# Optimization experiments

Hardware: AMD Instinct MI355X
Metric: run time of the kernel (lower is better)

The kernel has to match this reference:

```python
import jax, jax.numpy as jnp
import numpy as np

B, S, D_MODEL, H = 2, 2048, 1024, 16
HD = D_MODEL // H  # head_dim = 64


def setup_inputs() -> dict:
    key = jax.random.key(0)
    kx, kq, kk, kv, ko = jax.random.split(key, 5)
    scale = 1.0 / np.sqrt(D_MODEL)
    return {
        "x": jax.random.normal(kx, (B, S, D_MODEL), dtype=jnp.float32),
        "Wq": jax.random.normal(kq, (D_MODEL, D_MODEL), dtype=jnp.float32) * scale,
        "Wk": jax.random.normal(kk, (D_MODEL, D_MODEL), dtype=jnp.float32) * scale,
        "Wv": jax.random.normal(kv, (D_MODEL, D_MODEL), dtype=jnp.float32) * scale,
        "Wo": jax.random.normal(ko, (D_MODEL, D_MODEL), dtype=jnp.float32) * scale,
        "bo": jnp.zeros((D_MODEL,), dtype=jnp.float32),
    }


def reference(x, Wq, Wk, Wv, Wo, bo):
    b, s, _ = x.shape
    # project and split heads: [b, h, s, hd]
    q = (x @ Wq).reshape(b, s, H, HD).transpose(0, 2, 1, 3)
    k = (x @ Wk).reshape(b, s, H, HD).transpose(0, 2, 1, 3)
    v = (x @ Wv).reshape(b, s, H, HD).transpose(0, 2, 1, 3)
    # full attn score materialization, as in the original module
    scores = jnp.einsum("bhqd,bhkd->bhqk", q, k)
    causal = jnp.triu(jnp.ones((s, s), dtype=bool), k=1)  # True above diagonal -> masked
    scores = jnp.where(causal, -jnp.inf, scores)
    attn = jax.nn.softmax(scores / np.sqrt(HD), axis=-1)  # dropout p=0.0 (eval)
    ctx = jnp.einsum("bhqk,bhkd->bqhd", attn, v).reshape(b, s, D_MODEL)
    return ctx @ Wo + bo
```

## Files before the change

kernel.cpp:

```cpp
#include <hip/hip_runtime.h>
#include <stdint.h>

typedef __bf16 bf16x8 __attribute__((ext_vector_type(8)));
typedef float f32x4 __attribute__((ext_vector_type(4)));

static constexpr int B_ = 2, S_ = 2048, D_ = 1024, H_ = 16, HD_ = 64;
static constexpr int M_ = B_ * S_;
static constexpr size_t HSZ = (size_t)B_ * H_ * S_ * HD_;

#define DEV_INLINE __device__ __forceinline__

#define SC2F (0.125f * 1.4426950408889634f)

DEV_INLINE uint16_t f2bf(float f) {
  __bf16 h = (__bf16)f;
  return __builtin_bit_cast(uint16_t, h);
}
DEV_INLINE float bf2f(uint16_t u) {
  uint32_t x = (uint32_t)u << 16;
  return __builtin_bit_cast(float, x);
}
DEV_INLINE float fmax3(float a, float b, float c) { return fmaxf(fmaxf(a, b), c); }

#define GLD16(gptr, lptr)                                                        \
  __builtin_amdgcn_global_load_lds(                                              \
      (const __attribute__((address_space(1))) void*)(gptr),                     \
      (__attribute__((address_space(3))) void*)(lptr), 16, 0, 0)

__global__ void cvt_x_kernel(const float* __restrict__ x, uint16_t* __restrict__ xb) {
  int i = blockIdx.x * 256 + threadIdx.x;
  float4 v = reinterpret_cast<const float4*>(x)[i];
  ushort4 o;
  o.x = f2bf(v.x); o.y = f2bf(v.y); o.z = f2bf(v.z); o.w = f2bf(v.w);
  reinterpret_cast<ushort4*>(xb)[i] = o;
}

__global__ void tr_w_kernel(const float* __restrict__ W0, const float* __restrict__ W1,
                            const float* __restrict__ W2, const float* __restrict__ W3,
                            uint16_t* __restrict__ Wt) {
  __shared__ float tile[32][33];
  const float* W = (blockIdx.z == 0) ? W0 : (blockIdx.z == 1) ? W1
                   : (blockIdx.z == 2) ? W2 : W3;
  uint16_t* dst = Wt + (size_t)blockIdx.z * D_ * D_;
  int c = blockIdx.x * 32 + threadIdx.x;
  int r0 = blockIdx.y * 32;
#pragma unroll
  for (int j = threadIdx.y; j < 32; j += 8)
    tile[j][threadIdx.x] = W[(size_t)(r0 + j) * D_ + c];
  __syncthreads();
  int oc = blockIdx.y * 32 + threadIdx.x;
  int or0 = blockIdx.x * 32;
#pragma unroll
  for (int j = threadIdx.y; j < 32; j += 8)
    dst[(size_t)(or0 + j) * D_ + oc] = f2bf(tile[threadIdx.x][j]);
}

template <int EPI, int BM, int MINW>
__global__ __launch_bounds__(256, MINW)
void gemm_bt_kernel(const uint16_t* __restrict__ A, const uint16_t* __restrict__ Bt,
                    uint16_t* __restrict__ Cb, float* __restrict__ Cf,
                    const float* __restrict__ bias, int K, int gx, int chunk) {
  constexpr int MR = BM / 32;
  __shared__ uint16_t ldsA[2][BM * 32];
  __shared__ uint16_t ldsB[2][128 * 32];
  const int tid = threadIdx.x;
  const int lane = tid & 63;
  const int wid = tid >> 6;
  const int lo = lane & 15, hi = lane >> 4;

  const int id = blockIdx.x;
  const int tilei = (id & 7) * chunk + (id >> 3);
  const int bx = tilei % gx, by = tilei / gx;
  const int row0 = by * BM, col0 = bx * 128;
  const int wr = (wid >> 1) * (BM / 2), wc = (wid & 1) * 64;

  const uint16_t* gA = A + (size_t)(row0 + (tid >> 2)) * K + (tid & 3) * 8;
  const uint16_t* gB = Bt + (size_t)(col0 + (tid >> 2)) * K + (tid & 3) * 8;

  f32x4 acc[MR][4] = {};

  auto stage = [&](int kt, int buf) {
    const uint16_t* a = gA + kt * 32;
    const uint16_t* b = gB + kt * 32;
    char* la = (char*)&ldsA[buf][0] + tid * 16;
    char* lb = (char*)&ldsB[buf][0] + tid * 16;
    GLD16(a, la);
    if constexpr (BM == 128) GLD16(a + (size_t)64 * K, la + 4096);
    GLD16(b, lb);
    GLD16(b + (size_t)64 * K, lb + 4096);
  };

  const int nk = K >> 5;
  stage(0, 0);
  __syncthreads();
  for (int kt = 0; kt < nk; ++kt) {
    const int cur = kt & 1;
    if (kt + 1 < nk) stage(kt + 1, cur ^ 1);
    const uint16_t* lA = &ldsA[cur][0];
    const uint16_t* lB = &ldsB[cur][0];
    bf16x8 af[MR], bfr[4];
#pragma unroll
    for (int m = 0; m < MR; ++m)
      af[m] = *(const bf16x8*)(lA + (wr + m * 16 + lo) * 32 + hi * 8);
#pragma unroll
    for (int n = 0; n < 4; ++n)
      bfr[n] = *(const bf16x8*)(lB + (wc + n * 16 + lo) * 32 + hi * 8);
    __builtin_amdgcn_s_setprio(1);
#pragma unroll
    for (int m = 0; m < MR; ++m)
#pragma unroll
      for (int n = 0; n < 4; ++n)
        acc[m][n] = __builtin_amdgcn_mfma_f32_16x16x32_bf16(af[m], bfr[n], acc[m][n], 0, 0, 0);
    __builtin_amdgcn_s_setprio(0);
    __syncthreads();
  }

#pragma unroll
  for (int m = 0; m < MR; ++m)
#pragma unroll
    for (int n = 0; n < 4; ++n) {
      const int gr0 = row0 + wr + m * 16 + hi * 4;
      const int gc = col0 + wc + n * 16 + lo;
      if (EPI == 0) {
        const int which = gc >> 10, c = gc & 1023;
        const int hh = c >> 6, d = c & 63;
        const int bb = gr0 >> 11, s0 = gr0 & 2047;
        if (which == 2) {
          ushort4 pk;
          pk.x = f2bf(acc[m][n][0]); pk.y = f2bf(acc[m][n][1]);
          pk.z = f2bf(acc[m][n][2]); pk.w = f2bf(acc[m][n][3]);
          *reinterpret_cast<ushort4*>(
              &Cb[2 * HSZ + ((size_t)(bb * H_ + hh) * HD_ + d) * S_ + s0]) = pk;
        } else {
          const float qs = (which == 0) ? SC2F : 1.0f;
#pragma unroll
          for (int j = 0; j < 4; ++j)
            Cb[(size_t)which * HSZ + (((size_t)(bb * H_ + hh) * S_ + s0 + j) * HD_ + d)] =
                f2bf(acc[m][n][j] * qs);
        }
      } else {
#pragma unroll
        for (int j = 0; j < 4; ++j)
          Cf[(size_t)(gr0 + j) * D_ + gc] = acc[m][n][j] + bias[gc];
      }
    }
}

__global__ __launch_bounds__(256, 3)
void attn_kernel(const uint16_t* __restrict__ QKV, uint16_t* __restrict__ ctx,
                 uint16_t* __restrict__ Opart, float2* __restrict__ ml) {
  __shared__ uint16_t ldsKV[2][2][4096];
  __shared__ uint16_t ldsP[128][72];

  static const uint8_t jt[3][8] = {
      {0 << 2, 1 << 2, 2 << 2, 3 << 2, 4 << 2, 5 << 2, 6 << 2, (9 << 2) | 3},
      {(15 << 2) | 2, 7 << 2, (14 << 2) | 2, (14 << 2) | 3,
       (13 << 2) | 3, (12 << 2) | 3, (10 << 2) | 3, (11 << 2) | 2},
      {(15 << 2) | 3, (13 << 2) | 2, (12 << 2) | 2, (10 << 2) | 2,
       (9 << 2) | 2, (8 << 2) | 2, (8 << 2) | 3, (11 << 2) | 3},
  };

  const int tid = threadIdx.x;
  const int lane = tid & 63;
  const int w = tid >> 6;
  const int lo = lane & 15, hi = lane >> 4;
  const int swz = (hi * 8) ^ ((lo & 6) << 2);

  const int g = blockIdx.x;
  const int bh = g & 31, k = (g >> 5) & 7, r = g >> 8;
  const int j = jt[r][k];
  const int p = j >> 2;
  const bool split = (j & 2) != 0;
  const int c = j & 1;
  const int k0 = (split && c) ? (p + 1) : 0;
  const int k1 = (split && !c) ? (p + 1) : (2 * p + 2);
  const int h = bh & 15, b = bh >> 4;

  const size_t bhs = ((size_t)(b * H_ + h)) * S_ * HD_;
  const uint16_t* Q  = QKV + bhs;
  const uint16_t* Kp = QKV + HSZ + bhs;
  const uint16_t* Vt = QKV + 2 * HSZ + bhs;

  bf16x8 ones;
#pragma unroll
  for (int e = 0; e < 8; ++e) ones[e] = __builtin_bit_cast(__bf16, (uint16_t)0x3F80);

  const int srow = tid >> 2;
  const int scol = ((tid & 3) ^ ((tid >> 3) & 3)) * 8;
  auto stage = [&](int kt, int bufi) {
    const uint16_t* gk = Kp + (size_t)(kt * 64 + srow) * HD_ + scol;
    char* lk = (char*)&ldsKV[bufi][0][0] + tid * 16;
    GLD16(gk, lk);
    GLD16(gk + 32, lk + 4096);
    const uint16_t* gv = Vt + (size_t)srow * S_ + kt * 64 + scol;
    char* lv = (char*)&ldsKV[bufi][1][0] + tid * 16;
    GLD16(gv, lv);
    GLD16(gv + 32, lv + 4096);
  };

  const int q0w = p * 128 + w * 32;
  bf16x8 qf[2][2];
#pragma unroll
  for (int mm = 0; mm < 2; ++mm)
#pragma unroll
    for (int ks = 0; ks < 2; ++ks)
      qf[mm][ks] = *(const bf16x8*)(Q + (size_t)(q0w + mm * 16 + lo) * HD_ + ks * 32 + hi * 8);

  f32x4 acco[2][4] = {};
  f32x4 lacc[2] = {};
  float mstate[2] = {-1e30f, -1e30f};

  stage(k0, k0 & 1);
  asm volatile("s_waitcnt vmcnt(0)" ::: "memory");
  __builtin_amdgcn_s_barrier();
  __builtin_amdgcn_sched_barrier(0);

  for (int kt = k0; kt < k1; ++kt) {
    const int buf = kt & 1;
    if (kt + 1 < k1) stage(kt + 1, buf ^ 1);

    const bool active = (kt * 64) < (q0w + 32);
    if (active) {
      const uint16_t* lK = &ldsKV[buf][0][0];
      bf16x8 ak[4][2];
#pragma unroll
      for (int n = 0; n < 4; ++n)
#pragma unroll
        for (int ks = 0; ks < 2; ++ks)
          ak[n][ks] = *(const bf16x8*)(lK + ks * 2048 + (n * 16 + lo) * 32 + swz);

      f32x4 st[4][2];
      __builtin_amdgcn_s_setprio(1);
#pragma unroll
      for (int n = 0; n < 4; ++n)
#pragma unroll
        for (int mm = 0; mm < 2; ++mm) {
          f32x4 z = {};
          z = __builtin_amdgcn_mfma_f32_16x16x32_bf16(ak[n][0], qf[mm][0], z, 0, 0, 0);
          st[n][mm] = __builtin_amdgcn_mfma_f32_16x16x32_bf16(ak[n][1], qf[mm][1], z, 0, 0, 0);
        }
      __builtin_amdgcn_s_setprio(0);

      if (kt * 64 + 63 > q0w) {
#pragma unroll
        for (int n = 0; n < 4; ++n)
#pragma unroll
          for (int mm = 0; mm < 2; ++mm) {
            const int qg = q0w + mm * 16 + lo;
#pragma unroll
            for (int jj = 0; jj < 4; ++jj) {
              int kvg = kt * 64 + n * 16 + hi * 4 + jj;
              if (kvg > qg) st[n][mm][jj] = -1e30f;
            }
          }
      }

#pragma unroll
      for (int mm = 0; mm < 2; ++mm) {
        float t0 = fmax3(st[0][mm][0], st[0][mm][1], st[0][mm][2]);
        float t1 = fmax3(t0, st[0][mm][3], st[1][mm][0]);
        float t2 = fmax3(t1, st[1][mm][1], st[1][mm][2]);
        float t3 = fmax3(t2, st[1][mm][3], st[2][mm][0]);
        float t4 = fmax3(t3, st[2][mm][1], st[2][mm][2]);
        float t5 = fmax3(t4, st[2][mm][3], st[3][mm][0]);
        float t6 = fmax3(t5, st[3][mm][1], st[3][mm][2]);
        float vmax = fmaxf(t6, st[3][mm][3]);
        vmax = fmaxf(vmax, __shfl_xor(vmax, 16));
        vmax = fmaxf(vmax, __shfl_xor(vmax, 32));

        if (__any(vmax > mstate[mm] + 8.f)) {
          float mnew = fmaxf(mstate[mm], vmax);
          float sc = exp2f(mstate[mm] - mnew);
          mstate[mm] = mnew;
          lacc[mm] *= sc;
#pragma unroll
          for (int nd = 0; nd < 4; ++nd)
#pragma unroll
            for (int jj = 0; jj < 4; ++jj) acco[mm][nd][jj] *= sc;
        }

#pragma unroll
        for (int n = 0; n < 4; ++n) {
          ushort4 pk;
          pk.x = f2bf(exp2f(st[n][mm][0] - mstate[mm]));
          pk.y = f2bf(exp2f(st[n][mm][1] - mstate[mm]));
          pk.z = f2bf(exp2f(st[n][mm][2] - mstate[mm]));
          pk.w = f2bf(exp2f(st[n][mm][3] - mstate[mm]));
          *reinterpret_cast<ushort4*>(&ldsP[w * 32 + mm * 16 + lo][n * 16 + hi * 4]) = pk;
        }
      }

      const uint16_t* lV = &ldsKV[buf][1][0];
      bf16x8 ap[2][2], bv[4][2];
#pragma unroll
      for (int mm = 0; mm < 2; ++mm)
#pragma unroll
        for (int ks = 0; ks < 2; ++ks)
          ap[mm][ks] = *(const bf16x8*)(&ldsP[w * 32 + mm * 16 + lo][ks * 32 + hi * 8]);
#pragma unroll
      for (int nd = 0; nd < 4; ++nd)
#pragma unroll
        for (int ks = 0; ks < 2; ++ks)
          bv[nd][ks] = *(const bf16x8*)(lV + ks * 2048 + (nd * 16 + lo) * 32 + swz);
      __builtin_amdgcn_s_setprio(1);
#pragma unroll
      for (int mm = 0; mm < 2; ++mm) {
        lacc[mm] = __builtin_amdgcn_mfma_f32_16x16x32_bf16(ones, ap[mm][0], lacc[mm], 0, 0, 0);
        lacc[mm] = __builtin_amdgcn_mfma_f32_16x16x32_bf16(ones, ap[mm][1], lacc[mm], 0, 0, 0);
#pragma unroll
        for (int nd = 0; nd < 4; ++nd) {
          acco[mm][nd] = __builtin_amdgcn_mfma_f32_16x16x32_bf16(bv[nd][0], ap[mm][0], acco[mm][nd], 0, 0, 0);
          acco[mm][nd] = __builtin_amdgcn_mfma_f32_16x16x32_bf16(bv[nd][1], ap[mm][1], acco[mm][nd], 0, 0, 0);
        }
      }
      __builtin_amdgcn_s_setprio(0);
    }

    asm volatile("s_waitcnt vmcnt(0)" ::: "memory");
    __builtin_amdgcn_s_barrier();
    __builtin_amdgcn_sched_barrier(0);
  }

  if (!split) {
#pragma unroll
    for (int mm = 0; mm < 2; ++mm) {
      const float inv = 1.f / lacc[mm][0];
      uint16_t* crow = ctx + (size_t)(b * S_ + q0w + mm * 16 + lo) * D_ + h * HD_;
#pragma unroll
      for (int nd = 0; nd < 4; ++nd) {
        ushort4 pk;
        pk.x = f2bf(acco[mm][nd][0] * inv); pk.y = f2bf(acco[mm][nd][1] * inv);
        pk.z = f2bf(acco[mm][nd][2] * inv); pk.w = f2bf(acco[mm][nd][3] * inv);
        *reinterpret_cast<ushort4*>(crow + nd * 16 + hi * 4) = pk;
      }
    }
  } else {
    const int idx = ((bh * 8) + (p - 8)) * 2 + c;
    uint16_t* op = Opart + (size_t)idx * 8192;
#pragma unroll
    for (int mm = 0; mm < 2; ++mm) {
      const int qloc = w * 32 + mm * 16 + lo;
#pragma unroll
      for (int nd = 0; nd < 4; ++nd) {
        ushort4 pk;
        pk.x = f2bf(acco[mm][nd][0]); pk.y = f2bf(acco[mm][nd][1]);
        pk.z = f2bf(acco[mm][nd][2]); pk.w = f2bf(acco[mm][nd][3]);
        *reinterpret_cast<ushort4*>(op + qloc * 64 + nd * 16 + hi * 4) = pk;
      }
      if (hi == 0) ml[idx * 128 + qloc] = make_float2(mstate[mm], lacc[mm][0]);
    }
  }
}

__global__ void merge_kernel(const uint16_t* __restrict__ Opart,
                             const float2* __restrict__ ml,
                             uint16_t* __restrict__ ctx) {
  const int t = blockIdx.x * 256 + threadIdx.x;
  const int dh = t & 3, row = t >> 2;
  const int q = row & 127, si = (row >> 7) & 7, bh = row >> 10;
  const int h = bh & 15, b = bh >> 4;
  const int p = 8 + si;
  const int base = (bh * 8 + si) * 2;

  const float2 A = ml[base * 128 + q];
  const float2 Bv = ml[base * 128 + 128 + q];
  const float m = fmaxf(A.x, Bv.x);
  float sa = exp2f(A.x - m), sb = exp2f(Bv.x - m);
  const float inv = 1.f / (A.y * sa + Bv.y * sb);
  sa *= inv; sb *= inv;

  const uint16_t* Oa = Opart + (size_t)base * 8192 + q * 64 + dh * 16;
  const uint16_t* Ob = Oa + 8192;
  uint16_t* pc = ctx + ((size_t)(b * S_) + p * 128 + q) * D_ + h * HD_ + dh * 16;
#pragma unroll
  for (int hf = 0; hf < 2; ++hf) {
    int4 va = ((const int4*)Oa)[hf], vb = ((const int4*)Ob)[hf];
    const uint16_t* ua = (const uint16_t*)&va;
    const uint16_t* ub = (const uint16_t*)&vb;
    int4 vo;
    uint16_t* uo = (uint16_t*)&vo;
#pragma unroll
    for (int i = 0; i < 8; ++i)
      uo[i] = f2bf(bf2f(ua[i]) * sa + bf2f(ub[i]) * sb);
    ((int4*)pc)[hf] = vo;
  }
}

extern "C" void kernel_launch(void* const* d_in, const int* in_sizes, int n_in,
                              void* d_out, int out_size, void* d_ws, size_t ws_size,
                              hipStream_t stream) {
  (void)in_sizes; (void)n_in; (void)out_size; (void)ws_size;
  const float* x  = (const float*)d_in[0];
  const float* Wq = (const float*)d_in[1];
  const float* Wk = (const float*)d_in[2];
  const float* Wv = (const float*)d_in[3];
  const float* Wo = (const float*)d_in[4];
  const float* bo = (const float*)d_in[5];
  float* out = (float*)d_out;

  uint16_t* ws  = (uint16_t*)d_ws;
  uint16_t* xb  = ws;
  uint16_t* Wt  = xb + (size_t)M_ * D_;
  uint16_t* QKV = Wt + (size_t)4 * D_ * D_;
  uint16_t* ctx = QKV + 3 * HSZ;
  uint16_t* Opart = xb;
  float2*   mlbuf = (float2*)Wt;

  cvt_x_kernel<<<(M_ * D_) / 1024, 256, 0, stream>>>(x, xb);
  tr_w_kernel<<<dim3(32, 32, 4), dim3(32, 8), 0, stream>>>(Wq, Wk, Wv, Wo, Wt);
  gemm_bt_kernel<0, 128, 3><<<768, 256, 0, stream>>>(xb, Wt, QKV, nullptr, nullptr, D_, 24, 96);
  attn_kernel<<<768, 256, 0, stream>>>(QKV, ctx, Opart, mlbuf);
  merge_kernel<<<512, 256, 0, stream>>>(Opart, mlbuf, ctx);
  gemm_bt_kernel<1, 64, 2><<<512, 256, 0, stream>>>(ctx, Wt + (size_t)3 * D_ * D_, nullptr, out, bo, D_, 8, 64);
}
```

Measured before the change: 115.2 us.

## Split every attention query block into two KV halves and build P via shuffles

Every causal query block is now split into two equal-size KV ranges (1024 jobs instead of 768 mixed whole/split jobs), with a new job table and a merge over all blocks. The P matrix is assembled in registers via lane shuffles instead of an LDS round trip, and the row sum is computed with scalar adds plus shuffles instead of an extra MFMA against a ones vector. Occupancy hint is raised to 4 waves per SIMD thanks to the dropped LDS buffer. In exchange the merge kernel now processes every row, doubling its traffic, and partial outputs for all blocks go through bf16.

```diff
diff --git a/kernel.cpp b/kernel.cpp
--- a/kernel.cpp
+++ b/kernel.cpp
@@ -3,6 +3,7 @@
 
 typedef __bf16 bf16x8 __attribute__((ext_vector_type(8)));
 typedef float f32x4 __attribute__((ext_vector_type(4)));
+typedef uint32_t u32x4 __attribute__((ext_vector_type(4)));
 
 static constexpr int B_ = 2, S_ = 2048, D_ = 1024, H_ = 16, HD_ = 64;
 static constexpr int M_ = B_ * S_;
@@ -15,6 +16,9 @@
 DEV_INLINE uint16_t f2bf(float f) {
   __bf16 h = (__bf16)f;
   return __builtin_bit_cast(uint16_t, h);
+}
+DEV_INLINE uint32_t pack2bf(float a, float b) {
+  return (uint32_t)f2bf(a) | ((uint32_t)f2bf(b) << 16);
 }
 DEV_INLINE float bf2f(uint16_t u) {
   uint32_t x = (uint32_t)u << 16;
@@ -146,18 +150,16 @@
     }
 }
 
-__global__ __launch_bounds__(256, 3)
+__global__ __launch_bounds__(256, 4)
 void attn_kernel(const uint16_t* __restrict__ QKV, uint16_t* __restrict__ ctx,
                  uint16_t* __restrict__ Opart, float2* __restrict__ ml) {
   __shared__ uint16_t ldsKV[2][2][4096];
-  __shared__ uint16_t ldsP[128][72];
-
-  static const uint8_t jt[3][8] = {
-      {0 << 2, 1 << 2, 2 << 2, 3 << 2, 4 << 2, 5 << 2, 6 << 2, (9 << 2) | 3},
-      {(15 << 2) | 2, 7 << 2, (14 << 2) | 2, (14 << 2) | 3,
-       (13 << 2) | 3, (12 << 2) | 3, (10 << 2) | 3, (11 << 2) | 2},
-      {(15 << 2) | 3, (13 << 2) | 2, (12 << 2) | 2, (10 << 2) | 2,
-       (9 << 2) | 2, (8 << 2) | 2, (8 << 2) | 3, (11 << 2) | 3},
+
+  static const uint8_t jobtab[4][8] = {
+      {30, 0, 26, 4, 22, 8, 18, 12},
+      {28, 2, 24, 6, 20, 10, 16, 14},
+      {3, 29, 7, 25, 11, 21, 15, 17},
+      {1, 31, 5, 27, 9, 23, 13, 19},
   };
 
   const int tid = threadIdx.x;
@@ -167,23 +169,17 @@
   const int swz = (hi * 8) ^ ((lo & 6) << 2);
 
   const int g = blockIdx.x;
-  const int bh = g & 31, k = (g >> 5) & 7, r = g >> 8;
-  const int j = jt[r][k];
-  const int p = j >> 2;
-  const bool split = (j & 2) != 0;
-  const int c = j & 1;
-  const int k0 = (split && c) ? (p + 1) : 0;
-  const int k1 = (split && !c) ? (p + 1) : (2 * p + 2);
+  const int bh = g & 31, a = (g >> 5) & 7, r = g >> 8;
+  const int j = jobtab[r][a];
+  const int p = j >> 1, half = j & 1;
+  const int k0 = half ? (p + 1) : 0;
+  const int k1 = half ? (2 * p + 2) : (p + 1);
   const int h = bh & 15, b = bh >> 4;
 
   const size_t bhs = ((size_t)(b * H_ + h)) * S_ * HD_;
   const uint16_t* Q  = QKV + bhs;
   const uint16_t* Kp = QKV + HSZ + bhs;
   const uint16_t* Vt = QKV + 2 * HSZ + bhs;
-
-  bf16x8 ones;
-#pragma unroll
-  for (int e = 0; e < 8; ++e) ones[e] = __builtin_bit_cast(__bf16, (uint16_t)0x3F80);
 
   const int srow = tid >> 2;
   const int scol = ((tid & 3) ^ ((tid >> 3) & 3)) * 8;
@@ -207,8 +203,12 @@
       qf[mm][ks] = *(const bf16x8*)(Q + (size_t)(q0w + mm * 16 + lo) * HD_ + ks * 32 + hi * 8);
 
   f32x4 acco[2][4] = {};
-  f32x4 lacc[2] = {};
   float mstate[2] = {-1e30f, -1e30f};
+  float lstate[2] = {0.f, 0.f};
+
+  const int s1 = lo + ((hi & 1) << 5);
+  const int s2 = s1 + 16;
+  const bool hiSel = (hi >> 1) != 0;
 
   stage(k0, k0 & 1);
   asm volatile("s_waitcnt vmcnt(0)" ::: "memory");
@@ -255,6 +255,7 @@
           }
       }
 
+      bf16x8 ap[2][2];
 #pragma unroll
       for (int mm = 0; mm < 2; ++mm) {
         float t0 = fmax3(st[0][mm][0], st[0][mm][1], st[0][mm][2]);
@@ -272,31 +273,51 @@
           float mnew = fmaxf(mstate[mm], vmax);
           float sc = exp2f(mstate[mm] - mnew);
           mstate[mm] = mnew;
-          lacc[mm] *= sc;
+          lstate[mm] *= sc;
 #pragma unroll
           for (int nd = 0; nd < 4; ++nd)
 #pragma unroll
             for (int jj = 0; jj < 4; ++jj) acco[mm][nd][jj] *= sc;
         }
 
+        float pv[4][4];
+        float rsum = 0.f;
+#pragma unroll
+        for (int n = 0; n < 4; ++n)
+#pragma unroll
+          for (int jj = 0; jj < 4; ++jj) {
+            float e = exp2f(st[n][mm][jj] - mstate[mm]);
+            pv[n][jj] = e;
+            rsum += e;
+          }
+        rsum += __shfl_xor(rsum, 16);
+        rsum += __shfl_xor(rsum, 32);
+        lstate[mm] += rsum;
+
+        uint32_t pk[4][2];
 #pragma unroll
         for (int n = 0; n < 4; ++n) {
-          ushort4 pk;
-          pk.x = f2bf(exp2f(st[n][mm][0] - mstate[mm]));
-          pk.y = f2bf(exp2f(st[n][mm][1] - mstate[mm]));
-          pk.z = f2bf(exp2f(st[n][mm][2] - mstate[mm]));
-          pk.w = f2bf(exp2f(st[n][mm][3] - mstate[mm]));
-          *reinterpret_cast<ushort4*>(&ldsP[w * 32 + mm * 16 + lo][n * 16 + hi * 4]) = pk;
+          pk[n][0] = pack2bf(pv[n][0], pv[n][1]);
+          pk[n][1] = pack2bf(pv[n][2], pv[n][3]);
+        }
+
+#pragma unroll
+        for (int ks = 0; ks < 2; ++ks) {
+          uint32_t w0a = __shfl((int)pk[2 * ks][0], s1), w0b = __shfl((int)pk[2 * ks + 1][0], s1);
+          uint32_t w1a = __shfl((int)pk[2 * ks][1], s1), w1b = __shfl((int)pk[2 * ks + 1][1], s1);
+          uint32_t w2a = __shfl((int)pk[2 * ks][0], s2), w2b = __shfl((int)pk[2 * ks + 1][0], s2);
+          uint32_t w3a = __shfl((int)pk[2 * ks][1], s2), w3b = __shfl((int)pk[2 * ks + 1][1], s2);
+          u32x4 v;
+          v.x = hiSel ? w0b : w0a;
+          v.y = hiSel ? w1b : w1a;
+          v.z = hiSel ? w2b : w2a;
+          v.w = hiSel ? w3b : w3a;
+          ap[mm][ks] = __builtin_bit_cast(bf16x8, v);
         }
       }
 
       const uint16_t* lV = &ldsKV[buf][1][0];
-      bf16x8 ap[2][2], bv[4][2];
-#pragma unroll
-      for (int mm = 0; mm < 2; ++mm)
-#pragma unroll
-        for (int ks = 0; ks < 2; ++ks)
-          ap[mm][ks] = *(const bf16x8*)(&ldsP[w * 32 + mm * 16 + lo][ks * 32 + hi * 8]);
+      bf16x8 bv[4][2];
 #pragma unroll
       for (int nd = 0; nd < 4; ++nd)
 #pragma unroll
@@ -304,15 +325,12 @@
           bv[nd][ks] = *(const bf16x8*)(lV + ks * 2048 + (nd * 16 + lo) * 32 + swz);
       __builtin_amdgcn_s_setprio(1);
 #pragma unroll
-      for (int mm = 0; mm < 2; ++mm) {
-        lacc[mm] = __builtin_amdgcn_mfma_f32_16x16x32_bf16(ones, ap[mm][0], lacc[mm], 0, 0, 0);
-        lacc[mm] = __builtin_amdgcn_mfma_f32_16x16x32_bf16(ones, ap[mm][1], lacc[mm], 0, 0, 0);
+      for (int mm = 0; mm < 2; ++mm)
 #pragma unroll
         for (int nd = 0; nd < 4; ++nd) {
           acco[mm][nd] = __builtin_amdgcn_mfma_f32_16x16x32_bf16(bv[nd][0], ap[mm][0], acco[mm][nd], 0, 0, 0);
           acco[mm][nd] = __builtin_amdgcn_mfma_f32_16x16x32_bf16(bv[nd][1], ap[mm][1], acco[mm][nd], 0, 0, 0);
         }
-      }
       __builtin_amdgcn_s_setprio(0);
     }
 
@@ -321,34 +339,23 @@
     __builtin_amdgcn_sched_barrier(0);
   }
 
-  if (!split) {
-#pragma unroll
-    for (int mm = 0; mm < 2; ++mm) {
-      const float inv = 1.f / lacc[mm][0];
-      uint16_t* crow = ctx + (size_t)(b * S_ + q0w + mm * 16 + lo) * D_ + h * HD_;
-#pragma unroll
-      for (int nd = 0; nd < 4; ++nd) {
-        ushort4 pk;
-        pk.x = f2bf(acco[mm][nd][0] * inv); pk.y = f2bf(acco[mm][nd][1] * inv);
-        pk.z = f2bf(acco[mm][nd][2] * inv); pk.w = f2bf(acco[mm][nd][3] * inv);
-        *reinterpret_cast<ushort4*>(crow + nd * 16 + hi * 4) = pk;
-      }
+#pragma unroll
+  for (int mm = 0; mm < 2; ++mm) {
+    const int qloc = w * 32 + mm * 16 + lo;
+    uint16_t* dst;
+    if (half == 0)
+      dst = ctx + (size_t)(b * S_ + p * 128 + qloc) * D_ + h * HD_;
+    else
+      dst = Opart + (size_t)(bh * 16 + p) * 8192 + (size_t)qloc * 64;
+#pragma unroll
+    for (int nd = 0; nd < 4; ++nd) {
+      ushort4 pko;
+      pko.x = f2bf(acco[mm][nd][0]); pko.y = f2bf(acco[mm][nd][1]);
+      pko.z = f2bf(acco[mm][nd][2]); pko.w = f2bf(acco[mm][nd][3]);
+      *reinterpret_cast<ushort4*>(dst + nd * 16 + hi * 4) = pko;
     }
-  } else {
-    const int idx = ((bh * 8) + (p - 8)) * 2 + c;
-    uint16_t* op = Opart + (size_t)idx * 8192;
-#pragma unroll
-    for (int mm = 0; mm < 2; ++mm) {
-      const int qloc = w * 32 + mm * 16 + lo;
-#pragma unroll
-      for (int nd = 0; nd < 4; ++nd) {
-        ushort4 pk;
-        pk.x = f2bf(acco[mm][nd][0]); pk.y = f2bf(acco[mm][nd][1]);
-        pk.z = f2bf(acco[mm][nd][2]); pk.w = f2bf(acco[mm][nd][3]);
-        *reinterpret_cast<ushort4*>(op + qloc * 64 + nd * 16 + hi * 4) = pk;
-      }
-      if (hi == 0) ml[idx * 128 + qloc] = make_float2(mstate[mm], lacc[mm][0]);
-    }
+    if (hi == 0)
+      ml[((bh * 16 + p) * 2 + half) * 128 + qloc] = make_float2(mstate[mm], lstate[mm]);
   }
 }
 
@@ -357,24 +364,22 @@
                              uint16_t* __restrict__ ctx) {
   const int t = blockIdx.x * 256 + threadIdx.x;
   const int dh = t & 3, row = t >> 2;
-  const int q = row & 127, si = (row >> 7) & 7, bh = row >> 10;
+  const int q = row & 127, p = (row >> 7) & 15, bh = row >> 11;
   const int h = bh & 15, b = bh >> 4;
-  const int p = 8 + si;
-  const int base = (bh * 8 + si) * 2;
+  const int base = (bh * 16 + p) * 2;
 
   const float2 A = ml[base * 128 + q];
-  const float2 Bv = ml[base * 128 + 128 + q];
+  const float2 Bv = ml[(base + 1) * 128 + q];
   const float m = fmaxf(A.x, Bv.x);
   float sa = exp2f(A.x - m), sb = exp2f(Bv.x - m);
   const float inv = 1.f / (A.y * sa + Bv.y * sb);
   sa *= inv; sb *= inv;
 
-  const uint16_t* Oa = Opart + (size_t)base * 8192 + q * 64 + dh * 16;
-  const uint16_t* Ob = Oa + 8192;
   uint16_t* pc = ctx + ((size_t)(b * S_) + p * 128 + q) * D_ + h * HD_ + dh * 16;
+  const uint16_t* pb = Opart + (size_t)(bh * 16 + p) * 8192 + (size_t)q * 64 + dh * 16;
 #pragma unroll
   for (int hf = 0; hf < 2; ++hf) {
-    int4 va = ((const int4*)Oa)[hf], vb = ((const int4*)Ob)[hf];
+    int4 va = ((const int4*)pc)[hf], vb = ((const int4*)pb)[hf];
     const uint16_t* ua = (const uint16_t*)&va;
     const uint16_t* ub = (const uint16_t*)&vb;
     int4 vo;
@@ -409,7 +414,7 @@
   cvt_x_kernel<<<(M_ * D_) / 1024, 256, 0, stream>>>(x, xb);
   tr_w_kernel<<<dim3(32, 32, 4), dim3(32, 8), 0, stream>>>(Wq, Wk, Wv, Wo, Wt);
   gemm_bt_kernel<0, 128, 3><<<768, 256, 0, stream>>>(xb, Wt, QKV, nullptr, nullptr, D_, 24, 96);
-  attn_kernel<<<768, 256, 0, stream>>>(QKV, ctx, Opart, mlbuf);
-  merge_kernel<<<512, 256, 0, stream>>>(Opart, mlbuf, ctx);
+  attn_kernel<<<1024, 256, 0, stream>>>(QKV, ctx, Opart, mlbuf);
+  merge_kernel<<<1024, 256, 0, stream>>>(Opart, mlbuf, ctx);
   gemm_bt_kernel<1, 64, 2><<<512, 256, 0, stream>>>(ctx, Wt + (size_t)3 * D_ * D_, nullptr, out, bo, D_, 8, 64);
 }
```

After: 126.1 us. 1.09x slower.
